# Kernel optimization log

Measured on AMD Instinct MI355X. Metric: run time of the kernel, lower is better.

The kernel has to match this reference:

```python
import jax, jax.numpy as jnp
import numpy as np

N = 100000
E = 1600000
D = 128      # in_features
H = 128      # mlp hidden = out_features
O = 128      # out_features
BN_EPS = 1e-5

def _bn_train(x, gamma, beta):
    # BatchNorm1d in training mode: batch stats over node axis, biased variance
    mu = jnp.mean(x, axis=0)
    var = jnp.mean((x - mu) ** 2, axis=0)
    return (x - mu) * jax.lax.rsqrt(var + BN_EPS) * gamma + beta

def setup_inputs() -> dict:
    key = jax.random.key(0)
    ks = jax.random.split(key, 8)
    h = jax.random.normal(ks[0], (N, D), dtype=jnp.float32)
    edge_src = jax.random.randint(ks[1], (E,), 0, N, dtype=jnp.int32)
    edge_dst = jax.random.randint(ks[2], (E,), 0, N, dtype=jnp.int32)
    s1 = 1.0 / np.sqrt(D)
    s2 = 1.0 / np.sqrt(H)
    W1 = jax.random.uniform(ks[3], (D, H), jnp.float32, -s1, s1)
    b1 = jax.random.uniform(ks[4], (H,), jnp.float32, -s1, s1)
    W2 = jax.random.uniform(ks[5], (H, O), jnp.float32, -s2, s2)
    b2 = jax.random.uniform(ks[6], (O,), jnp.float32, -s2, s2)
    return {
        "h": h, "edge_src": edge_src, "edge_dst": edge_dst,
        "W1": W1, "b1": b1, "g1": jnp.ones((H,), jnp.float32), "be1": jnp.zeros((H,), jnp.float32),
        "W2": W2, "b2": b2, "g2": jnp.ones((O,), jnp.float32), "be2": jnp.zeros((O,), jnp.float32),
        "eps": jnp.zeros((), jnp.float32),
    }

def reference(h, edge_src, edge_dst, W1, b1, g1, be1, W2, b2, g2, be2, eps):
    # spmm(Adj, h) == scatter-add of gathered neighbor features
    msgs = h[edge_src]                                   # [E, D] irregular gather
    pooled = jax.ops.segment_sum(msgs, edge_dst, num_segments=N)  # [N, D]
    pooled = pooled + (1.0 + eps) * h                    # eps combine
    # MLP (2 layers): Linear -> BN -> ReLU -> Linear
    x = jax.nn.relu(_bn_train(pooled @ W1 + b1, g1, be1))
    x = x @ W2 + b2
    # final BN + ReLU
    return jax.nn.relu(_bn_train(x, g2, be2))
```

## Files before the change

kernel.cpp:

```cpp
#include <hip/hip_runtime.h>
#include <hip/hip_bf16.h>
#include <stdint.h>

#define BN_EPS 1e-5f
#define NSTRIPE 64

typedef __attribute__((ext_vector_type(8)))  short bf16x8;
typedef __attribute__((ext_vector_type(16))) float f32x16;

static __device__ __forceinline__ float bflo2f(uint32_t p){
  union { uint32_t u; float f; } c; c.u = p << 16; return c.f;
}
static __device__ __forceinline__ float bfhi2f(uint32_t p){
  union { uint32_t u; float f; } c; c.u = p & 0xffff0000u; return c.f;
}
static __device__ __forceinline__ uint16_t f2bf(float f){
  union { float f; uint32_t u; } c; c.f = f;
  uint32_t u = c.u;
  return (uint16_t)((u + 0x7fffu + ((u >> 16) & 1u)) >> 16);
}
static __device__ __forceinline__ uint32_t pack2(float a, float b){
  return (uint32_t)f2bf(a) | ((uint32_t)f2bf(b) << 16);
}

__global__ void k_prep(const float* __restrict__ h, uint16_t* __restrict__ hb, int hblocks,
                       const float* __restrict__ W1, const float* __restrict__ W2,
                       uint16_t* __restrict__ Wt1, uint16_t* __restrict__ Wt2,
                       float* __restrict__ stats,
                       const int* __restrict__ dst, int* __restrict__ M, int E, int NB){
  int b = blockIdx.x, t = threadIdx.x;
  if (b < hblocks){
    int i = (b * 256 + t) * 8;
    float4 a = *(const float4*)(h + i);
    float4 bb = *(const float4*)(h + i + 4);
    uint4 o;
    o.x = pack2(a.x, a.y); o.y = pack2(a.z, a.w);
    o.z = pack2(bb.x, bb.y); o.w = pack2(bb.z, bb.w);
    *(uint4*)(hb + i) = o;
    return;
  }
  if (b < hblocks + 16){
    int gid = (b - hblocks) * 256 + t;
    {
      float4 z = make_float4(0.f, 0.f, 0.f, 0.f);
      *(float4*)(stats + gid * 8) = z;
      *(float4*)(stats + gid * 8 + 4) = z;
    }
    const float* Wf = (gid < 2048) ? W1 : W2;
    uint16_t* Wt = (gid < 2048) ? Wt1 : Wt2;
    int cid = gid & 2047;
    int nrow = cid >> 4;
    int c    = cid & 15;
    int k0 = c * 8;
    float e[8];
    #pragma unroll
    for (int j = 0; j < 8; ++j) e[j] = Wf[(k0 + j) * 128 + nrow];
    uint4 o;
    o.x = pack2(e[0], e[1]); o.y = pack2(e[2], e[3]);
    o.z = pack2(e[4], e[5]); o.w = pack2(e[6], e[7]);
    *(uint4*)(Wt + nrow * 128 + c * 8) = o;
    return;
  }
  int eb = b - hblocks - 16;
  __shared__ int cnt[512];
  cnt[t] = 0; cnt[t + 256] = 0;
  __syncthreads();
  int base = eb * 4096;
  #pragma unroll 4
  for (int j = t; j < 4096; j += 256){
    int i = base + j;
    if (i < E) atomicAdd(&cnt[dst[i] >> 8], 1);
  }
  __syncthreads();
  size_t row = (size_t)eb * NB;
  if (t < NB) M[row + t] = cnt[t];
  int t2 = t + 256;
  if (t2 < NB) M[row + t2] = cnt[t2];
}

__global__ void k_colscan(int* __restrict__ M, int* __restrict__ btot, int EB, int NB){
  __shared__ int s[256];
  int b = blockIdx.x, t = threadIdx.x;
  int i0 = 2 * t, i1 = 2 * t + 1;
  int v0 = (i0 < EB) ? M[(size_t)i0 * NB + b] : 0;
  int v1 = (i1 < EB) ? M[(size_t)i1 * NB + b] : 0;
  s[t] = v0 + v1;
  __syncthreads();
  for (int off = 1; off < 256; off <<= 1){
    int v = (t >= off) ? s[t - off] : 0;
    __syncthreads();
    s[t] += v;
    __syncthreads();
  }
  int excl = s[t] - (v0 + v1);
  if (i0 < EB) M[(size_t)i0 * NB + b] = excl;
  if (i1 < EB) M[(size_t)i1 * NB + b] = excl + v0;
  if (t == 255) btot[b] = s[255];
}

__global__ void k_bscan(const int* __restrict__ btot, int* __restrict__ bbase,
                        int* __restrict__ row_off, int NB, int n, int E){
  __shared__ int s[256];
  int t = threadIdx.x;
  int i0 = 2 * t, i1 = 2 * t + 1;
  int v0 = (i0 < NB) ? btot[i0] : 0;
  int v1 = (i1 < NB) ? btot[i1] : 0;
  s[t] = v0 + v1;
  __syncthreads();
  for (int off = 1; off < 256; off <<= 1){
    int v = (t >= off) ? s[t - off] : 0;
    __syncthreads();
    s[t] += v;
    __syncthreads();
  }
  int excl = s[t] - (v0 + v1);
  if (i0 < NB) bbase[i0] = excl;
  if (i1 < NB) bbase[i1] = excl + v0;
  if (t == 0){ bbase[NB] = E; row_off[n] = E; }
}

__global__ void k_bin(const int* __restrict__ src, const int* __restrict__ dst,
                      const int* __restrict__ M, const int* __restrict__ bbase,
                      uint32_t* __restrict__ binned, int E, int NB){
  __shared__ int comb[512];
  __shared__ int cur[512];
  int t = threadIdx.x;
  size_t row = (size_t)blockIdx.x * NB;
  if (t < NB) comb[t] = bbase[t] + M[row + t];
  int t2 = t + 256;
  if (t2 < NB) comb[t2] = bbase[t2] + M[row + t2];
  cur[t] = 0; cur[t + 256] = 0;
  __syncthreads();
  int base = blockIdx.x * 4096;
  #pragma unroll 4
  for (int j = t; j < 4096; j += 256){
    int i = base + j;
    if (i < E){
      int d = dst[i];
      int b = d >> 8;
      int r = atomicAdd(&cur[b], 1);
      binned[comb[b] + r] = (uint32_t)src[i] | ((uint32_t)(d & 255) << 24);
    }
  }
}

__global__ void k_csr(const uint32_t* __restrict__ binned, const int* __restrict__ bbase,
                      int* __restrict__ row_off, int* __restrict__ col_idx, int n){
  __shared__ int cnt[256];
  __shared__ int off[256];
  __shared__ int cur[256];
  int b = blockIdx.x, t = threadIdx.x;
  int e0 = bbase[b], e1 = bbase[b + 1];
  int nb0 = b << 8;
  cnt[t] = 0; cur[t] = 0;
  __syncthreads();
  int m = e1 - e0;
  for (int j = t; j < m; j += 256) atomicAdd(&cnt[binned[e0 + j] >> 24], 1);
  __syncthreads();
  int v = cnt[t];
  off[t] = v;
  __syncthreads();
  for (int o = 1; o < 256; o <<= 1){
    int u = (t >= o) ? off[t - o] : 0;
    __syncthreads();
    off[t] += u;
    __syncthreads();
  }
  int excl = off[t] - v;
  __syncthreads();
  off[t] = excl;
  if (nb0 + t < n) row_off[nb0 + t] = e0 + excl;
  __syncthreads();
  for (int j = t; j < m; j += 256){
    uint32_t p = binned[e0 + j];
    int dl = (int)(p >> 24);
    int r = atomicAdd(&cur[dl], 1);
    col_idx[e0 + off[dl] + r] = (int)(p & 0xFFFFFFu);
  }
}

__global__ __launch_bounds__(256, 4) void k_gg(
    const uint16_t* __restrict__ hb, const int* __restrict__ row_off,
    const int* __restrict__ col_idx, const float* __restrict__ eps_p,
    const uint16_t* __restrict__ Wt, const float* __restrict__ bias_f,
    uint16_t* __restrict__ Yout, float* __restrict__ osum_s, float* __restrict__ osq_s, int n){
  __shared__ __align__(16) uint16_t Al[64 * 128];
  __shared__ float csum[128], csq[128];
  int tid = threadIdx.x;
  int rbase = blockIdx.x * 64;
  int stripe = blockIdx.x & (NSTRIPE - 1);
  int grp = tid >> 4;
  int c   = tid & 15;
  const uint4* hp4 = (const uint4*)hb;
  float ce = 1.0f + eps_p[0];
  if (tid < 128){ csum[tid] = 0.f; csq[tid] = 0.f; }

  for (int it = 0; it < 4; ++it){
    int m = it * 16 + grp;
    int gr = rbase + m;
    float a0=0.f,a1=0.f,a2=0.f,a3=0.f,a4=0.f,a5=0.f,a6=0.f,a7=0.f;
    if (gr < n){
      int j = row_off[gr], jend = row_off[gr + 1];
      for (; j + 8 <= jend; j += 8){
        int s[8];
        #pragma unroll
        for (int e = 0; e < 8; ++e) s[e] = col_idx[j + e];
        uint4 v[8];
        #pragma unroll
        for (int e = 0; e < 8; ++e) v[e] = hp4[(size_t)s[e] * 16 + c];
        #pragma unroll
        for (int e = 0; e < 8; ++e){
          a0 += bflo2f(v[e].x); a1 += bfhi2f(v[e].x);
          a2 += bflo2f(v[e].y); a3 += bfhi2f(v[e].y);
          a4 += bflo2f(v[e].z); a5 += bfhi2f(v[e].z);
          a6 += bflo2f(v[e].w); a7 += bfhi2f(v[e].w);
        }
      }
      if (j < jend){
        int s[8]; float wq[8];
        #pragma unroll
        for (int e = 0; e < 8; ++e){
          int jj = j + e;
          wq[e] = (jj < jend) ? 1.f : 0.f;
          s[e] = col_idx[(jj < jend) ? jj : (jend - 1)];
        }
        uint4 v[8];
        #pragma unroll
        for (int e = 0; e < 8; ++e) v[e] = hp4[(size_t)s[e] * 16 + c];
        #pragma unroll
        for (int e = 0; e < 8; ++e){
          a0 = fmaf(wq[e], bflo2f(v[e].x), a0); a1 = fmaf(wq[e], bfhi2f(v[e].x), a1);
          a2 = fmaf(wq[e], bflo2f(v[e].y), a2); a3 = fmaf(wq[e], bfhi2f(v[e].y), a3);
          a4 = fmaf(wq[e], bflo2f(v[e].z), a4); a5 = fmaf(wq[e], bfhi2f(v[e].z), a5);
          a6 = fmaf(wq[e], bflo2f(v[e].w), a6); a7 = fmaf(wq[e], bfhi2f(v[e].w), a7);
        }
      }
      uint4 vh = hp4[(size_t)gr * 16 + c];
      a0 = fmaf(ce, bflo2f(vh.x), a0); a1 = fmaf(ce, bfhi2f(vh.x), a1);
      a2 = fmaf(ce, bflo2f(vh.y), a2); a3 = fmaf(ce, bfhi2f(vh.y), a3);
      a4 = fmaf(ce, bflo2f(vh.z), a4); a5 = fmaf(ce, bfhi2f(vh.z), a5);
      a6 = fmaf(ce, bflo2f(vh.w), a6); a7 = fmaf(ce, bfhi2f(vh.w), a7);
    }
    uint4 o;
    o.x = pack2(a0, a1); o.y = pack2(a2, a3);
    o.z = pack2(a4, a5); o.w = pack2(a6, a7);
    *(uint4*)((char*)Al + m * 256 + ((c ^ (m & 15)) * 16)) = o;
  }
  __syncthreads();

  int lane = tid & 63;
  int w    = tid >> 6;
  int hi   = lane >> 5;
  int key  = lane & 15;
  int m0   = (w & 1) * 32;
  int n0   = (w >> 1) * 64;
  int mrow = m0 + (lane & 31);
  int nrow0 = n0 + (lane & 31);
  int nrow1 = nrow0 + 32;

  f32x16 acc0, acc1;
  #pragma unroll
  for (int i = 0; i < 16; ++i){ acc0[i] = 0.f; acc1[i] = 0.f; }

  const char* Ab = (const char*)Al;
  #pragma unroll
  for (int kt = 0; kt < 8; ++kt){
    int ck = 2 * kt + hi;
    bf16x8 a  = *(const bf16x8*)(Ab + mrow * 256 + ((ck ^ key) * 16));
    bf16x8 b0 = *(const bf16x8*)(Wt + nrow0 * 128 + ck * 8);
    bf16x8 b1 = *(const bf16x8*)(Wt + nrow1 * 128 + ck * 8);
    acc0 = __builtin_amdgcn_mfma_f32_32x32x16_bf16(a, b0, acc0, 0, 0, 0);
    acc1 = __builtin_amdgcn_mfma_f32_32x32x16_bf16(a, b1, acc1, 0, 0, 0);
  }
  __syncthreads();

  uint16_t* Yl = Al;
  float bias0 = bias_f[nrow0];
  float bias1 = bias_f[nrow1];
  float ps0 = 0.f, pq0 = 0.f, ps1 = 0.f, pq1 = 0.f;
  #pragma unroll
  for (int r = 0; r < 16; ++r){
    int row = m0 + (r & 3) + 8 * (r >> 2) + 4 * hi;
    bool valid = (rbase + row) < n;
    float y0 = acc0[r] + bias0;
    float y1 = acc1[r] + bias1;
    if (valid){
      ps0 += y0; pq0 += y0 * y0;
      ps1 += y1; pq1 += y1 * y1;
    }
    Yl[row * 128 + nrow0] = f2bf(y0);
    Yl[row * 128 + nrow1] = f2bf(y1);
  }
  atomicAdd(&csum[nrow0], ps0); atomicAdd(&csq[nrow0], pq0);
  atomicAdd(&csum[nrow1], ps1); atomicAdd(&csq[nrow1], pq1);
  __syncthreads();

  #pragma unroll
  for (int i = 0; i < 4; ++i){
    int id = tid + 256 * i;
    int row = id >> 4, cc = id & 15;
    int gr = rbase + row;
    if (gr < n)
      *((uint4*)Yout + (size_t)gr * 16 + cc) = *((const uint4*)Yl + id);
  }
  if (tid < 128){
    atomicAdd(&osum_s[stripe * 128 + tid], csum[tid]);
    atomicAdd(&osq_s[stripe * 128 + tid], csq[tid]);
  }
}

__global__ __launch_bounds__(256, 4) void k_mgemm2(
    const uint16_t* __restrict__ Ag, const uint16_t* __restrict__ Wt,
    const float* __restrict__ bias_f,
    const float* __restrict__ sin_s, const float* __restrict__ sqin_s,
    const float* __restrict__ gin, const float* __restrict__ bein, float invN,
    uint16_t* __restrict__ Yout, float* __restrict__ osum_s, float* __restrict__ osq_s, int n){
  __shared__ __align__(16) uint16_t Al[64 * 128];
  __shared__ float csum[128], csq[128];
  __shared__ __align__(16) float ABl[256];
  int tid = threadIdx.x;
  int rbase = blockIdx.x * 64;
  int stripe = blockIdx.x & (NSTRIPE - 1);

  if (tid < 128){
    float s = 0.f, q = 0.f;
    #pragma unroll 8
    for (int st = 0; st < NSTRIPE; ++st){
      s += sin_s[st * 128 + tid];
      q += sqin_s[st * 128 + tid];
    }
    float mu = s * invN;
    float var = q * invN - mu * mu;
    float A = gin[tid] * rsqrtf(var + BN_EPS);
    ABl[tid] = A;
    ABl[128 + tid] = bein[tid] - mu * A;
    csum[tid] = 0.f; csq[tid] = 0.f;
  }
  __syncthreads();

  #pragma unroll
  for (int i = 0; i < 4; ++i){
    int f = tid + 256 * i;
    int m = f >> 4, c = f & 15;
    int gr = rbase + m;
    uint4 v = make_uint4(0, 0, 0, 0);
    if (gr < n){
      v = *(const uint4*)(Ag + (size_t)gr * 128 + c * 8);
      int k0 = c * 8;
      float4 ka0 = *(const float4*)(ABl + k0);
      float4 ka1 = *(const float4*)(ABl + k0 + 4);
      float4 kb0 = *(const float4*)(ABl + 128 + k0);
      float4 kb1 = *(const float4*)(ABl + 128 + k0 + 4);
      float e0 = fmaxf(fmaf(bflo2f(v.x), ka0.x, kb0.x), 0.f);
      float e1 = fmaxf(fmaf(bfhi2f(v.x), ka0.y, kb0.y), 0.f);
      float e2 = fmaxf(fmaf(bflo2f(v.y), ka0.z, kb0.z), 0.f);
      float e3 = fmaxf(fmaf(bfhi2f(v.y), ka0.w, kb0.w), 0.f);
      float e4 = fmaxf(fmaf(bflo2f(v.z), ka1.x, kb1.x), 0.f);
      float e5 = fmaxf(fmaf(bfhi2f(v.z), ka1.y, kb1.y), 0.f);
      float e6 = fmaxf(fmaf(bflo2f(v.w), ka1.z, kb1.z), 0.f);
      float e7 = fmaxf(fmaf(bfhi2f(v.w), ka1.w, kb1.w), 0.f);
      v.x = pack2(e0, e1); v.y = pack2(e2, e3);
      v.z = pack2(e4, e5); v.w = pack2(e6, e7);
    }
    *(uint4*)((char*)Al + m * 256 + ((c ^ (m & 15)) * 16)) = v;
  }
  __syncthreads();

  int lane = tid & 63;
  int w    = tid >> 6;
  int hi   = lane >> 5;
  int key  = lane & 15;
  int m0   = (w & 1) * 32;
  int n0   = (w >> 1) * 64;
  int mrow = m0 + (lane & 31);
  int nrow0 = n0 + (lane & 31);
  int nrow1 = nrow0 + 32;

  f32x16 acc0, acc1;
  #pragma unroll
  for (int i = 0; i < 16; ++i){ acc0[i] = 0.f; acc1[i] = 0.f; }

  const char* Ab = (const char*)Al;
  #pragma unroll
  for (int kt = 0; kt < 8; ++kt){
    int ck = 2 * kt + hi;
    bf16x8 a  = *(const bf16x8*)(Ab + mrow * 256 + ((ck ^ key) * 16));
    bf16x8 b0 = *(const bf16x8*)(Wt + nrow0 * 128 + ck * 8);
    bf16x8 b1 = *(const bf16x8*)(Wt + nrow1 * 128 + ck * 8);
    acc0 = __builtin_amdgcn_mfma_f32_32x32x16_bf16(a, b0, acc0, 0, 0, 0);
    acc1 = __builtin_amdgcn_mfma_f32_32x32x16_bf16(a, b1, acc1, 0, 0, 0);
  }
  __syncthreads();

  uint16_t* Yl = Al;
  float bias0 = bias_f[nrow0];
  float bias1 = bias_f[nrow1];
  float ps0 = 0.f, pq0 = 0.f, ps1 = 0.f, pq1 = 0.f;
  #pragma unroll
  for (int r = 0; r < 16; ++r){
    int row = m0 + (r & 3) + 8 * (r >> 2) + 4 * hi;
    bool valid = (rbase + row) < n;
    float y0 = acc0[r] + bias0;
    float y1 = acc1[r] + bias1;
    if (valid){
      ps0 += y0; pq0 += y0 * y0;
      ps1 += y1; pq1 += y1 * y1;
    }
    Yl[row * 128 + nrow0] = f2bf(y0);
    Yl[row * 128 + nrow1] = f2bf(y1);
  }
  atomicAdd(&csum[nrow0], ps0); atomicAdd(&csq[nrow0], pq0);
  atomicAdd(&csum[nrow1], ps1); atomicAdd(&csq[nrow1], pq1);
  __syncthreads();

  #pragma unroll
  for (int i = 0; i < 4; ++i){
    int id = tid + 256 * i;
    int row = id >> 4, cc = id & 15;
    int gr = rbase + row;
    if (gr < n)
      *((uint4*)Yout + (size_t)gr * 16 + cc) = *((const uint4*)Yl + id);
  }
  if (tid < 128){
    atomicAdd(&osum_s[stripe * 128 + tid], csum[tid]);
    atomicAdd(&osq_s[stripe * 128 + tid], csq[tid]);
  }
}

__global__ void k_bncoef2(const float* __restrict__ sum_s, const float* __restrict__ sq_s,
                          const float* __restrict__ g, const float* __restrict__ be,
                          float* __restrict__ AB, float invN){
  int c = threadIdx.x;
  if (c < 128){
    float s = 0.f, q = 0.f;
    #pragma unroll 8
    for (int st = 0; st < NSTRIPE; ++st){
      s += sum_s[st * 128 + c];
      q += sq_s[st * 128 + c];
    }
    float mu = s * invN;
    float var = q * invN - mu * mu;
    float A = g[c] * rsqrtf(var + BN_EPS);
    AB[c] = A;
    AB[128 + c] = be[c] - mu * A;
  }
}

__global__ void k_final(const uint16_t* __restrict__ Y2b, const float* __restrict__ ABg,
                        float* __restrict__ out, int total){
  __shared__ __align__(16) float AB[256];
  int tid = threadIdx.x;
  if (tid < 64){
    *(float4*)(AB + tid * 4) = *(const float4*)(ABg + tid * 4);
  }
  __syncthreads();
  int i = (blockIdx.x * 256 + tid) * 4;
  if (i >= total) return;
  uint2 v = *(const uint2*)(Y2b + i);
  int c = i & 127;
  float4 a = *(const float4*)(AB + c);
  float4 b = *(const float4*)(AB + 128 + c);
  float4 o;
  o.x = fmaxf(fmaf(bflo2f(v.x), a.x, b.x), 0.f);
  o.y = fmaxf(fmaf(bfhi2f(v.x), a.y, b.y), 0.f);
  o.z = fmaxf(fmaf(bflo2f(v.y), a.z, b.z), 0.f);
  o.w = fmaxf(fmaf(bfhi2f(v.y), a.w, b.w), 0.f);
  *(float4*)(out + i) = o;
}

extern "C" void kernel_launch(void* const* d_in, const int* in_sizes, int n_in,
                              void* d_out, int out_size, void* d_ws, size_t ws_size,
                              hipStream_t stream){
  const float* h    = (const float*)d_in[0];
  const int*   esrc = (const int*)d_in[1];
  const int*   edst = (const int*)d_in[2];
  const float* W1   = (const float*)d_in[3];
  const float* b1   = (const float*)d_in[4];
  const float* g1   = (const float*)d_in[5];
  const float* be1  = (const float*)d_in[6];
  const float* W2   = (const float*)d_in[7];
  const float* b2   = (const float*)d_in[8];
  const float* g2   = (const float*)d_in[9];
  const float* be2  = (const float*)d_in[10];
  const float* eps  = (const float*)d_in[11];
  int n = in_sizes[0] / 128;
  int E = in_sizes[1];
  (void)n_in; (void)out_size; (void)ws_size;

  int NB = (n + 255) >> 8;
  int EB = (E + 4095) >> 12;

  char* ws = (char*)d_ws;
  size_t off = 0;
  auto alloc = [&](size_t bytes) -> void* {
    void* p = ws + off;
    off += (bytes + 511) & ~(size_t)511;
    return p;
  };
  size_t feat_b = (size_t)n * 128 * 2;
  uint16_t* B1   = (uint16_t*)alloc(feat_b);
  uint16_t* B2   = (uint16_t*)alloc(feat_b);
  int*   row_off = (int*)alloc((size_t)(n + 1) * 4);
  int*   col_idx = (int*)alloc((size_t)E * 4);
  int*   M       = (int*)alloc((size_t)EB * NB * 4);
  int*   btot    = (int*)alloc((size_t)(NB + 1) * 4);
  int*   bbase   = (int*)alloc((size_t)(NB + 1) * 4);
  float* stats   = (float*)alloc((size_t)4 * NSTRIPE * 128 * 4);
  float* AB2     = (float*)alloc(256 * 4);
  uint16_t* Wt1  = (uint16_t*)alloc(128 * 128 * 2);
  uint16_t* Wt2  = (uint16_t*)alloc(128 * 128 * 2);
  float* sum1 = stats;
  float* sq1  = stats + NSTRIPE * 128;
  float* sum2 = stats + 2 * NSTRIPE * 128;
  float* sq2  = stats + 3 * NSTRIPE * 128;
  uint16_t* hb  = B1;
  uint32_t* binned = (uint32_t*)B2;
  uint16_t* Y1b = B2;
  uint16_t* Y2b = B1;

  int total = n * 128;
  int hblocks = total / 8 / 256;
  float invN = 1.0f / (float)n;

  k_prep<<<hblocks + 16 + EB, 256, 0, stream>>>(h, hb, hblocks, W1, W2, Wt1, Wt2,
                                                stats, edst, M, E, NB);
  k_colscan<<<NB, 256, 0, stream>>>(M, btot, EB, NB);
  k_bscan  <<<1, 256, 0, stream>>>(btot, bbase, row_off, NB, n, E);
  k_bin    <<<EB, 256, 0, stream>>>(esrc, edst, M, bbase, binned, E, NB);
  k_csr    <<<NB, 256, 0, stream>>>(binned, bbase, row_off, col_idx, n);

  int gblocks = (n + 63) / 64;
  k_gg<<<gblocks, 256, 0, stream>>>(hb, row_off, col_idx, eps, Wt1, b1,
                                    Y1b, sum1, sq1, n);
  k_mgemm2<<<gblocks, 256, 0, stream>>>(Y1b, Wt2, b2,
      sum1, sq1, g1, be1, invN, Y2b, sum2, sq2, n);

  k_bncoef2<<<1, 128, 0, stream>>>(sum2, sq2, g2, be2, AB2, invN);
  k_final<<<(total / 4 + 255) / 256, 256, 0, stream>>>(Y2b, AB2, (float*)d_out, total);
}
```

Measured before the change: 300.4 us.

## Make gather-GEMM and second GEMM kernels persistent with an atomic tile counter

Both fused GEMM kernels now launch at most 1024 blocks, and each block loops, pulling 64-row tiles from a global atomic counter. The counters are zeroed in the prep kernel. BatchNorm partial sums accumulate in registers across all tiles a block handles, and are flushed to the striped global stats once per block instead of once per tile. The aim is to balance the uneven per-row gather cost dynamically, and to cut launch tail and global atomic traffic. In exchange it adds a per-tile atomic and barrier, and tile order now depends on timing.

```diff
diff --git a/kernel.cpp b/kernel.cpp
--- a/kernel.cpp
+++ b/kernel.cpp
@@ -26,7 +26,7 @@
 __global__ void k_prep(const float* __restrict__ h, uint16_t* __restrict__ hb, int hblocks,
                        const float* __restrict__ W1, const float* __restrict__ W2,
                        uint16_t* __restrict__ Wt1, uint16_t* __restrict__ Wt2,
-                       float* __restrict__ stats,
+                       float* __restrict__ stats, int* __restrict__ ctr,
                        const int* __restrict__ dst, int* __restrict__ M, int E, int NB){
   int b = blockIdx.x, t = threadIdx.x;
   if (b < hblocks){
@@ -41,6 +41,7 @@
   }
   if (b < hblocks + 16){
     int gid = (b - hblocks) * 256 + t;
+    if (gid == 0){ ctr[0] = 0; ctr[1] = 0; }
     {
       float4 z = make_float4(0.f, 0.f, 0.f, 0.f);
       *(float4*)(stats + gid * 8) = z;
@@ -183,70 +184,16 @@
     const uint16_t* __restrict__ hb, const int* __restrict__ row_off,
     const int* __restrict__ col_idx, const float* __restrict__ eps_p,
     const uint16_t* __restrict__ Wt, const float* __restrict__ bias_f,
-    uint16_t* __restrict__ Yout, float* __restrict__ osum_s, float* __restrict__ osq_s, int n){
+    uint16_t* __restrict__ Yout, float* __restrict__ osum_s, float* __restrict__ osq_s,
+    int* __restrict__ ctr, int ntiles, int n){
   __shared__ __align__(16) uint16_t Al[64 * 128];
   __shared__ float csum[128], csq[128];
+  __shared__ int tile_s;
   int tid = threadIdx.x;
-  int rbase = blockIdx.x * 64;
-  int stripe = blockIdx.x & (NSTRIPE - 1);
   int grp = tid >> 4;
   int c   = tid & 15;
   const uint4* hp4 = (const uint4*)hb;
   float ce = 1.0f + eps_p[0];
-  if (tid < 128){ csum[tid] = 0.f; csq[tid] = 0.f; }
-
-  for (int it = 0; it < 4; ++it){
-    int m = it * 16 + grp;
-    int gr = rbase + m;
-    float a0=0.f,a1=0.f,a2=0.f,a3=0.f,a4=0.f,a5=0.f,a6=0.f,a7=0.f;
-    if (gr < n){
-      int j = row_off[gr], jend = row_off[gr + 1];
-      for (; j + 8 <= jend; j += 8){
-        int s[8];
-        #pragma unroll
-        for (int e = 0; e < 8; ++e) s[e] = col_idx[j + e];
-        uint4 v[8];
-        #pragma unroll
-        for (int e = 0; e < 8; ++e) v[e] = hp4[(size_t)s[e] * 16 + c];
-        #pragma unroll
-        for (int e = 0; e < 8; ++e){
-          a0 += bflo2f(v[e].x); a1 += bfhi2f(v[e].x);
-          a2 += bflo2f(v[e].y); a3 += bfhi2f(v[e].y);
-          a4 += bflo2f(v[e].z); a5 += bfhi2f(v[e].z);
-          a6 += bflo2f(v[e].w); a7 += bfhi2f(v[e].w);
-        }
-      }
-      if (j < jend){
-        int s[8]; float wq[8];
-        #pragma unroll
-        for (int e = 0; e < 8; ++e){
-          int jj = j + e;
-          wq[e] = (jj < jend) ? 1.f : 0.f;
-          s[e] = col_idx[(jj < jend) ? jj : (jend - 1)];
-        }
-        uint4 v[8];
-        #pragma unroll
-        for (int e = 0; e < 8; ++e) v[e] = hp4[(size_t)s[e] * 16 + c];
-        #pragma unroll
-        for (int e = 0; e < 8; ++e){
-          a0 = fmaf(wq[e], bflo2f(v[e].x), a0); a1 = fmaf(wq[e], bfhi2f(v[e].x), a1);
-          a2 = fmaf(wq[e], bflo2f(v[e].y), a2); a3 = fmaf(wq[e], bfhi2f(v[e].y), a3);
-          a4 = fmaf(wq[e], bflo2f(v[e].z), a4); a5 = fmaf(wq[e], bfhi2f(v[e].z), a5);
-          a6 = fmaf(wq[e], bflo2f(v[e].w), a6); a7 = fmaf(wq[e], bfhi2f(v[e].w), a7);
-        }
-      }
-      uint4 vh = hp4[(size_t)gr * 16 + c];
-      a0 = fmaf(ce, bflo2f(vh.x), a0); a1 = fmaf(ce, bfhi2f(vh.x), a1);
-      a2 = fmaf(ce, bflo2f(vh.y), a2); a3 = fmaf(ce, bfhi2f(vh.y), a3);
-      a4 = fmaf(ce, bflo2f(vh.z), a4); a5 = fmaf(ce, bfhi2f(vh.z), a5);
-      a6 = fmaf(ce, bflo2f(vh.w), a6); a7 = fmaf(ce, bfhi2f(vh.w), a7);
-    }
-    uint4 o;
-    o.x = pack2(a0, a1); o.y = pack2(a2, a3);
-    o.z = pack2(a4, a5); o.w = pack2(a6, a7);
-    *(uint4*)((char*)Al + m * 256 + ((c ^ (m & 15)) * 16)) = o;
-  }
-  __syncthreads();
 
   int lane = tid & 63;
   int w    = tid >> 6;
@@ -257,52 +204,118 @@
   int mrow = m0 + (lane & 31);
   int nrow0 = n0 + (lane & 31);
   int nrow1 = nrow0 + 32;
-
-  f32x16 acc0, acc1;
-  #pragma unroll
-  for (int i = 0; i < 16; ++i){ acc0[i] = 0.f; acc1[i] = 0.f; }
-
-  const char* Ab = (const char*)Al;
-  #pragma unroll
-  for (int kt = 0; kt < 8; ++kt){
-    int ck = 2 * kt + hi;
-    bf16x8 a  = *(const bf16x8*)(Ab + mrow * 256 + ((ck ^ key) * 16));
-    bf16x8 b0 = *(const bf16x8*)(Wt + nrow0 * 128 + ck * 8);
-    bf16x8 b1 = *(const bf16x8*)(Wt + nrow1 * 128 + ck * 8);
-    acc0 = __builtin_amdgcn_mfma_f32_32x32x16_bf16(a, b0, acc0, 0, 0, 0);
-    acc1 = __builtin_amdgcn_mfma_f32_32x32x16_bf16(a, b1, acc1, 0, 0, 0);
-  }
-  __syncthreads();
-
-  uint16_t* Yl = Al;
   float bias0 = bias_f[nrow0];
   float bias1 = bias_f[nrow1];
   float ps0 = 0.f, pq0 = 0.f, ps1 = 0.f, pq1 = 0.f;
-  #pragma unroll
-  for (int r = 0; r < 16; ++r){
-    int row = m0 + (r & 3) + 8 * (r >> 2) + 4 * hi;
-    bool valid = (rbase + row) < n;
-    float y0 = acc0[r] + bias0;
-    float y1 = acc1[r] + bias1;
-    if (valid){
-      ps0 += y0; pq0 += y0 * y0;
-      ps1 += y1; pq1 += y1 * y1;
-    }
-    Yl[row * 128 + nrow0] = f2bf(y0);
-    Yl[row * 128 + nrow1] = f2bf(y1);
-  }
+
+  while (true){
+    if (tid == 0) tile_s = atomicAdd(ctr, 1);
+    __syncthreads();
+    int tile = tile_s;
+    if (tile >= ntiles) break;
+    int rbase = tile * 64;
+
+    for (int it = 0; it < 4; ++it){
+      int m = it * 16 + grp;
+      int gr = rbase + m;
+      float a0=0.f,a1=0.f,a2=0.f,a3=0.f,a4=0.f,a5=0.f,a6=0.f,a7=0.f;
+      if (gr < n){
+        int j = row_off[gr], jend = row_off[gr + 1];
+        for (; j + 8 <= jend; j += 8){
+          int s[8];
+          #pragma unroll
+          for (int e = 0; e < 8; ++e) s[e] = col_idx[j + e];
+          uint4 v[8];
+          #pragma unroll
+          for (int e = 0; e < 8; ++e) v[e] = hp4[(size_t)s[e] * 16 + c];
+          #pragma unroll
+          for (int e = 0; e < 8; ++e){
+            a0 += bflo2f(v[e].x); a1 += bfhi2f(v[e].x);
+            a2 += bflo2f(v[e].y); a3 += bfhi2f(v[e].y);
+            a4 += bflo2f(v[e].z); a5 += bfhi2f(v[e].z);
+            a6 += bflo2f(v[e].w); a7 += bfhi2f(v[e].w);
+          }
+        }
+        if (j < jend){
+          int s[8]; float wq[8];
+          #pragma unroll
+          for (int e = 0; e < 8; ++e){
+            int jj = j + e;
+            wq[e] = (jj < jend) ? 1.f : 0.f;
+            s[e] = col_idx[(jj < jend) ? jj : (jend - 1)];
+          }
+          uint4 v[8];
+          #pragma unroll
+          for (int e = 0; e < 8; ++e) v[e] = hp4[(size_t)s[e] * 16 + c];
+          #pragma unroll
+          for (int e = 0; e < 8; ++e){
+            a0 = fmaf(wq[e], bflo2f(v[e].x), a0); a1 = fmaf(wq[e], bfhi2f(v[e].x), a1);
+            a2 = fmaf(wq[e], bflo2f(v[e].y), a2); a3 = fmaf(wq[e], bfhi2f(v[e].y), a3);
+            a4 = fmaf(wq[e], bflo2f(v[e].z), a4); a5 = fmaf(wq[e], bfhi2f(v[e].z), a5);
+            a6 = fmaf(wq[e], bflo2f(v[e].w), a6); a7 = fmaf(wq[e], bfhi2f(v[e].w), a7);
+          }
+        }
+        uint4 vh = hp4[(size_t)gr * 16 + c];
+        a0 = fmaf(ce, bflo2f(vh.x), a0); a1 = fmaf(ce, bfhi2f(vh.x), a1);
+        a2 = fmaf(ce, bflo2f(vh.y), a2); a3 = fmaf(ce, bfhi2f(vh.y), a3);
+        a4 = fmaf(ce, bflo2f(vh.z), a4); a5 = fmaf(ce, bfhi2f(vh.z), a5);
+        a6 = fmaf(ce, bflo2f(vh.w), a6); a7 = fmaf(ce, bfhi2f(vh.w), a7);
+      }
+      uint4 o;
+      o.x = pack2(a0, a1); o.y = pack2(a2, a3);
+      o.z = pack2(a4, a5); o.w = pack2(a6, a7);
+      *(uint4*)((char*)Al + m * 256 + ((c ^ (m & 15)) * 16)) = o;
+    }
+    __syncthreads();
+
+    f32x16 acc0, acc1;
+    #pragma unroll
+    for (int i = 0; i < 16; ++i){ acc0[i] = 0.f; acc1[i] = 0.f; }
+
+    const char* Ab = (const char*)Al;
+    #pragma unroll
+    for (int kt = 0; kt < 8; ++kt){
+      int ck = 2 * kt + hi;
+      bf16x8 a  = *(const bf16x8*)(Ab + mrow * 256 + ((ck ^ key) * 16));
+      bf16x8 b0 = *(const bf16x8*)(Wt + nrow0 * 128 + ck * 8);
+      bf16x8 b1 = *(const bf16x8*)(Wt + nrow1 * 128 + ck * 8);
+      acc0 = __builtin_amdgcn_mfma_f32_32x32x16_bf16(a, b0, acc0, 0, 0, 0);
+      acc1 = __builtin_amdgcn_mfma_f32_32x32x16_bf16(a, b1, acc1, 0, 0, 0);
+    }
+    __syncthreads();
+
+    uint16_t* Yl = Al;
+    #pragma unroll
+    for (int r = 0; r < 16; ++r){
+      int row = m0 + (r & 3) + 8 * (r >> 2) + 4 * hi;
+      bool valid = (rbase + row) < n;
+      float y0 = acc0[r] + bias0;
+      float y1 = acc1[r] + bias1;
+      if (valid){
+        ps0 += y0; pq0 += y0 * y0;
+        ps1 += y1; pq1 += y1 * y1;
+      }
+      Yl[row * 128 + nrow0] = f2bf(y0);
+      Yl[row * 128 + nrow1] = f2bf(y1);
+    }
+    __syncthreads();
+
+    #pragma unroll
+    for (int i = 0; i < 4; ++i){
+      int id = tid + 256 * i;
+      int row = id >> 4, cc = id & 15;
+      int gr = rbase + row;
+      if (gr < n)
+        *((uint4*)Yout + (size_t)gr * 16 + cc) = *((const uint4*)Yl + id);
+    }
+  }
+
+  if (tid < 128){ csum[tid] = 0.f; csq[tid] = 0.f; }
+  __syncthreads();
   atomicAdd(&csum[nrow0], ps0); atomicAdd(&csq[nrow0], pq0);
   atomicAdd(&csum[nrow1], ps1); atomicAdd(&csq[nrow1], pq1);
   __syncthreads();
-
-  #pragma unroll
-  for (int i = 0; i < 4; ++i){
-    int id = tid + 256 * i;
-    int row = id >> 4, cc = id & 15;
-    int gr = rbase + row;
-    if (gr < n)
-      *((uint4*)Yout + (size_t)gr * 16 + cc) = *((const uint4*)Yl + id);
-  }
+  int stripe = blockIdx.x & (NSTRIPE - 1);
   if (tid < 128){
     atomicAdd(&osum_s[stripe * 128 + tid], csum[tid]);
     atomicAdd(&osq_s[stripe * 128 + tid], csq[tid]);
@@ -314,13 +327,13 @@
     const float* __restrict__ bias_f,
     const float* __restrict__ sin_s, const float* __restrict__ sqin_s,
     const float* __restrict__ gin, const float* __restrict__ bein, float invN,
-    uint16_t* __restrict__ Yout, float* __restrict__ osum_s, float* __restrict__ osq_s, int n){
+    uint16_t* __restrict__ Yout, float* __restrict__ osum_s, float* __restrict__ osq_s,
+    int* __restrict__ ctr, int ntiles, int n){
   __shared__ __align__(16) uint16_t Al[64 * 128];
   __shared__ float csum[128], csq[128];
   __shared__ __align__(16) float ABl[256];
+  __shared__ int tile_s;
   int tid = threadIdx.x;
-  int rbase = blockIdx.x * 64;
-  int stripe = blockIdx.x & (NSTRIPE - 1);
 
   if (tid < 128){
     float s = 0.f, q = 0.f;
@@ -334,37 +347,7 @@
     float A = gin[tid] * rsqrtf(var + BN_EPS);
     ABl[tid] = A;
     ABl[128 + tid] = bein[tid] - mu * A;
-    csum[tid] = 0.f; csq[tid] = 0.f;
-  }
-  __syncthreads();
-
-  #pragma unroll
-  for (int i = 0; i < 4; ++i){
-    int f = tid + 256 * i;
-    int m = f >> 4, c = f & 15;
-    int gr = rbase + m;
-    uint4 v = make_uint4(0, 0, 0, 0);
-    if (gr < n){
-      v = *(const uint4*)(Ag + (size_t)gr * 128 + c * 8);
-      int k0 = c * 8;
-      float4 ka0 = *(const float4*)(ABl + k0);
-      float4 ka1 = *(const float4*)(ABl + k0 + 4);
-      float4 kb0 = *(const float4*)(ABl + 128 + k0);
-      float4 kb1 = *(const float4*)(ABl + 128 + k0 + 4);
-      float e0 = fmaxf(fmaf(bflo2f(v.x), ka0.x, kb0.x), 0.f);
-      float e1 = fmaxf(fmaf(bfhi2f(v.x), ka0.y, kb0.y), 0.f);
-      float e2 = fmaxf(fmaf(bflo2f(v.y), ka0.z, kb0.z), 0.f);
-      float e3 = fmaxf(fmaf(bfhi2f(v.y), ka0.w, kb0.w), 0.f);
-      float e4 = fmaxf(fmaf(bflo2f(v.z), ka1.x, kb1.x), 0.f);
-      float e5 = fmaxf(fmaf(bfhi2f(v.z), ka1.y, kb1.y), 0.f);
-      float e6 = fmaxf(fmaf(bflo2f(v.w), ka1.z, kb1.z), 0.f);
-      float e7 = fmaxf(fmaf(bfhi2f(v.w), ka1.w, kb1.w), 0.f);
-      v.x = pack2(e0, e1); v.y = pack2(e2, e3);
-      v.z = pack2(e4, e5); v.w = pack2(e6, e7);
-    }
-    *(uint4*)((char*)Al + m * 256 + ((c ^ (m & 15)) * 16)) = v;
-  }
-  __syncthreads();
+  }
 
   int lane = tid & 63;
   int w    = tid >> 6;
@@ -375,52 +358,93 @@
   int mrow = m0 + (lane & 31);
   int nrow0 = n0 + (lane & 31);
   int nrow1 = nrow0 + 32;
-
-  f32x16 acc0, acc1;
-  #pragma unroll
-  for (int i = 0; i < 16; ++i){ acc0[i] = 0.f; acc1[i] = 0.f; }
-
-  const char* Ab = (const char*)Al;
-  #pragma unroll
-  for (int kt = 0; kt < 8; ++kt){
-    int ck = 2 * kt + hi;
-    bf16x8 a  = *(const bf16x8*)(Ab + mrow * 256 + ((ck ^ key) * 16));
-    bf16x8 b0 = *(const bf16x8*)(Wt + nrow0 * 128 + ck * 8);
-    bf16x8 b1 = *(const bf16x8*)(Wt + nrow1 * 128 + ck * 8);
-    acc0 = __builtin_amdgcn_mfma_f32_32x32x16_bf16(a, b0, acc0, 0, 0, 0);
-    acc1 = __builtin_amdgcn_mfma_f32_32x32x16_bf16(a, b1, acc1, 0, 0, 0);
-  }
-  __syncthreads();
-
-  uint16_t* Yl = Al;
   float bias0 = bias_f[nrow0];
   float bias1 = bias_f[nrow1];
   float ps0 = 0.f, pq0 = 0.f, ps1 = 0.f, pq1 = 0.f;
-  #pragma unroll
-  for (int r = 0; r < 16; ++r){
-    int row = m0 + (r & 3) + 8 * (r >> 2) + 4 * hi;
-    bool valid = (rbase + row) < n;
-    float y0 = acc0[r] + bias0;
-    float y1 = acc1[r] + bias1;
-    if (valid){
-      ps0 += y0; pq0 += y0 * y0;
-      ps1 += y1; pq1 += y1 * y1;
-    }
-    Yl[row * 128 + nrow0] = f2bf(y0);
-    Yl[row * 128 + nrow1] = f2bf(y1);
-  }
+
+  while (true){
+    if (tid == 0) tile_s = atomicAdd(ctr, 1);
+    __syncthreads();
+    int tile = tile_s;
+    if (tile >= ntiles) break;
+    int rbase = tile * 64;
+
+    #pragma unroll
+    for (int i = 0; i < 4; ++i){
+      int f = tid + 256 * i;
+      int m = f >> 4, c = f & 15;
+      int gr = rbase + m;
+      uint4 v = make_uint4(0, 0, 0, 0);
+      if (gr < n){
+        v = *(const uint4*)(Ag + (size_t)gr * 128 + c * 8);
+        int k0 = c * 8;
+        float4 ka0 = *(const float4*)(ABl + k0);
+        float4 ka1 = *(const float4*)(ABl + k0 + 4);
+        float4 kb0 = *(const float4*)(ABl + 128 + k0);
+        float4 kb1 = *(const float4*)(ABl + 128 + k0 + 4);
+        float e0 = fmaxf(fmaf(bflo2f(v.x), ka0.x, kb0.x), 0.f);
+        float e1 = fmaxf(fmaf(bfhi2f(v.x), ka0.y, kb0.y), 0.f);
+        float e2 = fmaxf(fmaf(bflo2f(v.y), ka0.z, kb0.z), 0.f);
+        float e3 = fmaxf(fmaf(bfhi2f(v.y), ka0.w, kb0.w), 0.f);
+        float e4 = fmaxf(fmaf(bflo2f(v.z), ka1.x, kb1.x), 0.f);
+        float e5 = fmaxf(fmaf(bfhi2f(v.z), ka1.y, kb1.y), 0.f);
+        float e6 = fmaxf(fmaf(bflo2f(v.w), ka1.z, kb1.z), 0.f);
+        float e7 = fmaxf(fmaf(bfhi2f(v.w), ka1.w, kb1.w), 0.f);
+        v.x = pack2(e0, e1); v.y = pack2(e2, e3);
+        v.z = pack2(e4, e5); v.w = pack2(e6, e7);
+      }
+      *(uint4*)((char*)Al + m * 256 + ((c ^ (m & 15)) * 16)) = v;
+    }
+    __syncthreads();
+
+    f32x16 acc0, acc1;
+    #pragma unroll
+    for (int i = 0; i < 16; ++i){ acc0[i] = 0.f; acc1[i] = 0.f; }
+
+    const char* Ab = (const char*)Al;
+    #pragma unroll
+    for (int kt = 0; kt < 8; ++kt){
+      int ck = 2 * kt + hi;
+      bf16x8 a  = *(const bf16x8*)(Ab + mrow * 256 + ((ck ^ key) * 16));
+      bf16x8 b0 = *(const bf16x8*)(Wt + nrow0 * 128 + ck * 8);
+      bf16x8 b1 = *(const bf16x8*)(Wt + nrow1 * 128 + ck * 8);
+      acc0 = __builtin_amdgcn_mfma_f32_32x32x16_bf16(a, b0, acc0, 0, 0, 0);
+      acc1 = __builtin_amdgcn_mfma_f32_32x32x16_bf16(a, b1, acc1, 0, 0, 0);
+    }
+    __syncthreads();
+
+    uint16_t* Yl = Al;
+    #pragma unroll
+    for (int r = 0; r < 16; ++r){
+      int row = m0 + (r & 3) + 8 * (r >> 2) + 4 * hi;
+      bool valid = (rbase + row) < n;
+      float y0 = acc0[r] + bias0;
+      float y1 = acc1[r] + bias1;
+      if (valid){
+        ps0 += y0; pq0 += y0 * y0;
+        ps1 += y1; pq1 += y1 * y1;
+      }
+      Yl[row * 128 + nrow0] = f2bf(y0);
+      Yl[row * 128 + nrow1] = f2bf(y1);
+    }
+    __syncthreads();
+
+    #pragma unroll
+    for (int i = 0; i < 4; ++i){
+      int id = tid + 256 * i;
+      int row = id >> 4, cc = id & 15;
+      int gr = rbase + row;
+      if (gr < n)
+        *((uint4*)Yout + (size_t)gr * 16 + cc) = *((const uint4*)Yl + id);
+    }
+  }
+
+  if (tid < 128){ csum[tid] = 0.f; csq[tid] = 0.f; }
+  __syncthreads();
   atomicAdd(&csum[nrow0], ps0); atomicAdd(&csq[nrow0], pq0);
   atomicAdd(&csum[nrow1], ps1); atomicAdd(&csq[nrow1], pq1);
   __syncthreads();
-
-  #pragma unroll
-  for (int i = 0; i < 4; ++i){
-    int id = tid + 256 * i;
-    int row = id >> 4, cc = id & 15;
-    int gr = rbase + row;
-    if (gr < n)
-      *((uint4*)Yout + (size_t)gr * 16 + cc) = *((const uint4*)Yl + id);
-  }
+  int stripe = blockIdx.x & (NSTRIPE - 1);
   if (tid < 128){
     atomicAdd(&osum_s[stripe * 128 + tid], csum[tid]);
     atomicAdd(&osq_s[stripe * 128 + tid], csq[tid]);
@@ -509,6 +533,7 @@
   float* AB2     = (float*)alloc(256 * 4);
   uint16_t* Wt1  = (uint16_t*)alloc(128 * 128 * 2);
   uint16_t* Wt2  = (uint16_t*)alloc(128 * 128 * 2);
+  int*   ctr     = (int*)alloc(8 * 4);
   float* sum1 = stats;
   float* sq1  = stats + NSTRIPE * 128;
   float* sum2 = stats + 2 * NSTRIPE * 128;
@@ -523,17 +548,18 @@
   float invN = 1.0f / (float)n;
 
   k_prep<<<hblocks + 16 + EB, 256, 0, stream>>>(h, hb, hblocks, W1, W2, Wt1, Wt2,
-                                                stats, edst, M, E, NB);
+                                                stats, ctr, edst, M, E, NB);
   k_colscan<<<NB, 256, 0, stream>>>(M, btot, EB, NB);
   k_bscan  <<<1, 256, 0, stream>>>(btot, bbase, row_off, NB, n, E);
   k_bin    <<<EB, 256, 0, stream>>>(esrc, edst, M, bbase, binned, E, NB);
   k_csr    <<<NB, 256, 0, stream>>>(binned, bbase, row_off, col_idx, n);
 
-  int gblocks = (n + 63) / 64;
-  k_gg<<<gblocks, 256, 0, stream>>>(hb, row_off, col_idx, eps, Wt1, b1,
-                                    Y1b, sum1, sq1, n);
-  k_mgemm2<<<gblocks, 256, 0, stream>>>(Y1b, Wt2, b2,
-      sum1, sq1, g1, be1, invN, Y2b, sum2, sq2, n);
+  int ntiles = (n + 63) / 64;
+  int pblocks = ntiles < 1024 ? ntiles : 1024;
+  k_gg<<<pblocks, 256, 0, stream>>>(hb, row_off, col_idx, eps, Wt1, b1,
+                                    Y1b, sum1, sq1, ctr, ntiles, n);
+  k_mgemm2<<<pblocks, 256, 0, stream>>>(Y1b, Wt2, b2,
+      sum1, sq1, g1, be1, invN, Y2b, sum2, sq2, ctr + 1, ntiles, n);
 
   k_bncoef2<<<1, 128, 0, stream>>>(sum2, sq2, g2, be2, AB2, invN);
   k_final<<<(total / 4 + 255) / 256, 256, 0, stream>>>(Y2b, AB2, (float*)d_out, total);
```

New measurement: 348.6 us. 1.16x slower.

## Merge block scans via last-block pattern and widen binning and final kernels

Applied to the files above, without the earlier changes.

The per-bucket column scan and the global bucket scan are fused into one kernel. The last block to finish, found with an atomic counter, performs the global scan, which removes a separate single-block launch. The h-to-bf16 conversion moves from the prep kernel into that scan kernel, so it overlaps with scan work. The bin and CSR kernels now run 512-thread blocks, and the final BN+ReLU kernel handles 8 elements per thread with 128-bit loads. The last-block handoff adds atomics and a fence, and the counter must be reset on every call.

```diff
diff --git a/kernel.cpp b/kernel.cpp
--- a/kernel.cpp
+++ b/kernel.cpp
@@ -23,24 +23,14 @@
   return (uint32_t)f2bf(a) | ((uint32_t)f2bf(b) << 16);
 }
 
-__global__ void k_prep(const float* __restrict__ h, uint16_t* __restrict__ hb, int hblocks,
-                       const float* __restrict__ W1, const float* __restrict__ W2,
+__global__ void k_pre0(const float* __restrict__ W1, const float* __restrict__ W2,
                        uint16_t* __restrict__ Wt1, uint16_t* __restrict__ Wt2,
-                       float* __restrict__ stats,
+                       float* __restrict__ stats, int* __restrict__ ctr,
                        const int* __restrict__ dst, int* __restrict__ M, int E, int NB){
   int b = blockIdx.x, t = threadIdx.x;
-  if (b < hblocks){
-    int i = (b * 256 + t) * 8;
-    float4 a = *(const float4*)(h + i);
-    float4 bb = *(const float4*)(h + i + 4);
-    uint4 o;
-    o.x = pack2(a.x, a.y); o.y = pack2(a.z, a.w);
-    o.z = pack2(bb.x, bb.y); o.w = pack2(bb.z, bb.w);
-    *(uint4*)(hb + i) = o;
-    return;
-  }
-  if (b < hblocks + 16){
-    int gid = (b - hblocks) * 256 + t;
+  if (b < 16){
+    int gid = b * 256 + t;
+    if (gid == 0){ ctr[0] = 0; ctr[1] = 0; }
     {
       float4 z = make_float4(0.f, 0.f, 0.f, 0.f);
       *(float4*)(stats + gid * 8) = z;
@@ -61,7 +51,7 @@
     *(uint4*)(Wt + nrow * 128 + c * 8) = o;
     return;
   }
-  int eb = b - hblocks - 16;
+  int eb = b - 16;
   __shared__ int cnt[512];
   cnt[t] = 0; cnt[t + 256] = 0;
   __syncthreads();
@@ -78,9 +68,23 @@
   if (t2 < NB) M[row + t2] = cnt[t2];
 }
 
-__global__ void k_colscan(int* __restrict__ M, int* __restrict__ btot, int EB, int NB){
+__global__ void k_scan(const float* __restrict__ h, uint16_t* __restrict__ hb,
+                       int* __restrict__ M, int* __restrict__ btot, int* __restrict__ bbase,
+                       int* __restrict__ row_off, int* __restrict__ done,
+                       int EB, int NB, int n, int E){
+  int b = blockIdx.x, t = threadIdx.x;
+  if (b >= NB){
+    int i = ((b - NB) * 256 + t) * 8;
+    float4 a = *(const float4*)(h + i);
+    float4 bb = *(const float4*)(h + i + 4);
+    uint4 o;
+    o.x = pack2(a.x, a.y); o.y = pack2(a.z, a.w);
+    o.z = pack2(bb.x, bb.y); o.w = pack2(bb.z, bb.w);
+    *(uint4*)(hb + i) = o;
+    return;
+  }
   __shared__ int s[256];
-  int b = blockIdx.x, t = threadIdx.x;
+  __shared__ int amlast;
   int i0 = 2 * t, i1 = 2 * t + 1;
   int v0 = (i0 < EB) ? M[(size_t)i0 * NB + b] : 0;
   int v1 = (i1 < EB) ? M[(size_t)i1 * NB + b] : 0;
@@ -95,17 +99,17 @@
   int excl = s[t] - (v0 + v1);
   if (i0 < EB) M[(size_t)i0 * NB + b] = excl;
   if (i1 < EB) M[(size_t)i1 * NB + b] = excl + v0;
-  if (t == 255) btot[b] = s[255];
-}
-
-__global__ void k_bscan(const int* __restrict__ btot, int* __restrict__ bbase,
-                        int* __restrict__ row_off, int NB, int n, int E){
-  __shared__ int s[256];
-  int t = threadIdx.x;
-  int i0 = 2 * t, i1 = 2 * t + 1;
-  int v0 = (i0 < NB) ? btot[i0] : 0;
-  int v1 = (i1 < NB) ? btot[i1] : 0;
-  s[t] = v0 + v1;
+  if (t == 255){
+    atomicExch(&btot[b], s[255]);
+    __threadfence();
+    amlast = (atomicAdd(done, 1) == NB - 1) ? 1 : 0;
+  }
+  __syncthreads();
+  if (!amlast) return;
+  int j0 = 2 * t, j1 = 2 * t + 1;
+  int w0 = (j0 < NB) ? atomicAdd(&btot[j0], 0) : 0;
+  int w1 = (j1 < NB) ? atomicAdd(&btot[j1], 0) : 0;
+  s[t] = w0 + w1;
   __syncthreads();
   for (int off = 1; off < 256; off <<= 1){
     int v = (t >= off) ? s[t - off] : 0;
@@ -113,9 +117,9 @@
     s[t] += v;
     __syncthreads();
   }
-  int excl = s[t] - (v0 + v1);
-  if (i0 < NB) bbase[i0] = excl;
-  if (i1 < NB) bbase[i1] = excl + v0;
+  int ex2 = s[t] - (w0 + w1);
+  if (j0 < NB) bbase[j0] = ex2;
+  if (j1 < NB) bbase[j1] = ex2 + w0;
   if (t == 0){ bbase[NB] = E; row_off[n] = E; }
 }
 
@@ -127,13 +131,11 @@
   int t = threadIdx.x;
   size_t row = (size_t)blockIdx.x * NB;
   if (t < NB) comb[t] = bbase[t] + M[row + t];
-  int t2 = t + 256;
-  if (t2 < NB) comb[t2] = bbase[t2] + M[row + t2];
-  cur[t] = 0; cur[t + 256] = 0;
+  cur[t] = 0;
   __syncthreads();
   int base = blockIdx.x * 4096;
   #pragma unroll 4
-  for (int j = t; j < 4096; j += 256){
+  for (int j = t; j < 4096; j += 512){
     int i = base + j;
     if (i < E){
       int d = dst[i];
@@ -152,26 +154,28 @@
   int b = blockIdx.x, t = threadIdx.x;
   int e0 = bbase[b], e1 = bbase[b + 1];
   int nb0 = b << 8;
-  cnt[t] = 0; cur[t] = 0;
+  if (t < 256){ cnt[t] = 0; cur[t] = 0; }
   __syncthreads();
   int m = e1 - e0;
-  for (int j = t; j < m; j += 256) atomicAdd(&cnt[binned[e0 + j] >> 24], 1);
-  __syncthreads();
-  int v = cnt[t];
-  off[t] = v;
+  for (int j = t; j < m; j += 512) atomicAdd(&cnt[binned[e0 + j] >> 24], 1);
+  __syncthreads();
+  int v = (t < 256) ? cnt[t] : 0;
+  if (t < 256) off[t] = v;
   __syncthreads();
   for (int o = 1; o < 256; o <<= 1){
-    int u = (t >= o) ? off[t - o] : 0;
+    int u = (t >= o && t < 256) ? off[t - o] : 0;
     __syncthreads();
-    off[t] += u;
+    if (t < 256) off[t] += u;
     __syncthreads();
   }
-  int excl = off[t] - v;
-  __syncthreads();
-  off[t] = excl;
-  if (nb0 + t < n) row_off[nb0 + t] = e0 + excl;
-  __syncthreads();
-  for (int j = t; j < m; j += 256){
+  int excl = (t < 256) ? (off[t] - v) : 0;
+  __syncthreads();
+  if (t < 256){
+    off[t] = excl;
+    if (nb0 + t < n) row_off[nb0 + t] = e0 + excl;
+  }
+  __syncthreads();
+  for (int j = t; j < m; j += 512){
     uint32_t p = binned[e0 + j];
     int dl = (int)(p >> 24);
     int r = atomicAdd(&cur[dl], 1);
@@ -454,18 +458,25 @@
     *(float4*)(AB + tid * 4) = *(const float4*)(ABg + tid * 4);
   }
   __syncthreads();
-  int i = (blockIdx.x * 256 + tid) * 4;
+  int i = (blockIdx.x * 256 + tid) * 8;
   if (i >= total) return;
-  uint2 v = *(const uint2*)(Y2b + i);
+  uint4 v = *(const uint4*)(Y2b + i);
   int c = i & 127;
-  float4 a = *(const float4*)(AB + c);
-  float4 b = *(const float4*)(AB + 128 + c);
-  float4 o;
-  o.x = fmaxf(fmaf(bflo2f(v.x), a.x, b.x), 0.f);
-  o.y = fmaxf(fmaf(bfhi2f(v.x), a.y, b.y), 0.f);
-  o.z = fmaxf(fmaf(bflo2f(v.y), a.z, b.z), 0.f);
-  o.w = fmaxf(fmaf(bfhi2f(v.y), a.w, b.w), 0.f);
-  *(float4*)(out + i) = o;
+  float4 a0 = *(const float4*)(AB + c);
+  float4 a1 = *(const float4*)(AB + c + 4);
+  float4 b0 = *(const float4*)(AB + 128 + c);
+  float4 b1 = *(const float4*)(AB + 128 + c + 4);
+  float4 o0, o1;
+  o0.x = fmaxf(fmaf(bflo2f(v.x), a0.x, b0.x), 0.f);
+  o0.y = fmaxf(fmaf(bfhi2f(v.x), a0.y, b0.y), 0.f);
+  o0.z = fmaxf(fmaf(bflo2f(v.y), a0.z, b0.z), 0.f);
+  o0.w = fmaxf(fmaf(bfhi2f(v.y), a0.w, b0.w), 0.f);
+  o1.x = fmaxf(fmaf(bflo2f(v.z), a1.x, b1.x), 0.f);
+  o1.y = fmaxf(fmaf(bfhi2f(v.z), a1.y, b1.y), 0.f);
+  o1.z = fmaxf(fmaf(bflo2f(v.w), a1.z, b1.z), 0.f);
+  o1.w = fmaxf(fmaf(bfhi2f(v.w), a1.w, b1.w), 0.f);
+  *(float4*)(out + i) = o0;
+  *(float4*)(out + i + 4) = o1;
 }
 
 extern "C" void kernel_launch(void* const* d_in, const int* in_sizes, int n_in,
@@ -509,6 +520,7 @@
   float* AB2     = (float*)alloc(256 * 4);
   uint16_t* Wt1  = (uint16_t*)alloc(128 * 128 * 2);
   uint16_t* Wt2  = (uint16_t*)alloc(128 * 128 * 2);
+  int*   ctr     = (int*)alloc(8 * 4);
   float* sum1 = stats;
   float* sq1  = stats + NSTRIPE * 128;
   float* sum2 = stats + 2 * NSTRIPE * 128;
@@ -522,12 +534,11 @@
   int hblocks = total / 8 / 256;
   float invN = 1.0f / (float)n;
 
-  k_prep<<<hblocks + 16 + EB, 256, 0, stream>>>(h, hb, hblocks, W1, W2, Wt1, Wt2,
-                                                stats, edst, M, E, NB);
-  k_colscan<<<NB, 256, 0, stream>>>(M, btot, EB, NB);
-  k_bscan  <<<1, 256, 0, stream>>>(btot, bbase, row_off, NB, n, E);
-  k_bin    <<<EB, 256, 0, stream>>>(esrc, edst, M, bbase, binned, E, NB);
-  k_csr    <<<NB, 256, 0, stream>>>(binned, bbase, row_off, col_idx, n);
+  k_pre0<<<16 + EB, 256, 0, stream>>>(W1, W2, Wt1, Wt2, stats, ctr, edst, M, E, NB);
+  k_scan<<<NB + hblocks, 256, 0, stream>>>(h, hb, M, btot, bbase, row_off, ctr,
+                                           EB, NB, n, E);
+  k_bin <<<EB, 512, 0, stream>>>(esrc, edst, M, bbase, binned, E, NB);
+  k_csr <<<NB, 512, 0, stream>>>(binned, bbase, row_off, col_idx, n);
 
   int gblocks = (n + 63) / 64;
   k_gg<<<gblocks, 256, 0, stream>>>(hb, row_off, col_idx, eps, Wt1, b1,
@@ -536,5 +547,5 @@
       sum1, sq1, g1, be1, invN, Y2b, sum2, sq2, n);
 
   k_bncoef2<<<1, 128, 0, stream>>>(sum2, sq2, g2, be2, AB2, invN);
-  k_final<<<(total / 4 + 255) / 256, 256, 0, stream>>>(Y2b, AB2, (float*)d_out, total);
-}
+  k_final<<<(total / 8 + 255) / 256, 256, 0, stream>>>(Y2b, AB2, (float*)d_out, total);
+}
```

Result: slower. 310.6 us (+3.4%).
